# Kernel optimization log

Hardware: AMD Instinct MI355X
Metric: run time of the kernel (lower is better)

Reference implementation:

```python
import jax, jax.numpy as jnp
import numpy as np

STRIDE = 4
EPS = 1e-12  # guards sqrt grad at exactly-zero distance (weight[0] is all zeros)


def rbf_conv(x, w, stride=STRIDE):
    # x: (N, 1, H, W); w: (O, kh, kw). Computes per-window cdist to all O
    # prototype filters, then gauss RBF with std = unbiased std of the (N, O)
    # distance matrix at each window position (matches torch.std(dist)).
    O, kh, kw = w.shape
    patches = jax.lax.conv_general_dilated_patches(
        x, (kh, kw), (stride, stride), 'VALID')      # (N, kh*kw, oh, ow)
    p = jnp.transpose(patches, (0, 2, 3, 1))          # (N, oh, ow, P)
    wf = w.reshape(O, -1)                              # (O, P)
    d2 = (jnp.sum(p * p, -1)[..., None] + jnp.sum(wf * wf, -1)
          - 2.0 * jnp.einsum('nhwp,op->nhwo', p, wf))
    dist = jnp.sqrt(jnp.maximum(d2, 0.0) + EPS)       # (N, oh, ow, O)
    std = jnp.std(dist, axis=(0, 3), ddof=1, keepdims=True)  # per window pos
    out = jnp.exp(-0.5 * (dist / std) ** 2)           # gauss RBF
    return jnp.transpose(out, (0, 3, 1, 2))           # (N, O, oh, ow)


def crelu(x, b):
    return x * (x >= b).astype(x.dtype)


def sfm(x, shape, next_kernel, filt, alpha0=0.9):
    # get_RM: (N, C, h_in, w_in) -> (B, h, w, C) regrouping, then alpha-weighted
    # patch pooling over `filt`, emitting (B*h'*w', 1, kh_next, kw_next).
    h, w = shape
    f0, f1 = filt
    C = x.shape[1]
    rm = jnp.transpose(x, (0, 2, 3, 1)).reshape(-1, h, w, C)
    seq = jnp.arange(f0 * f1, dtype=x.dtype)[::-1]       # flipped sequence
    alpha = jnp.tile((alpha0 ** seq).reshape(f0, f1), (h // f0, w // f1))
    out = rm * alpha[None, :, :, None]
    out = out.reshape(-1, h // f0, f0, w // f1, f1, C).mean(axis=(2, 4))
    return out.reshape(-1, 1, *next_kernel)


def channel_forward(xc, w1, w2, w3, w4, cb):
    y = rbf_conv(xc, w1)                       # (B, 100, 6, 6)
    y = crelu(y, cb[0])
    y = sfm(y, (6, 6), (10, 10), (2, 2))       # (B*9, 1, 10, 10)
    y = rbf_conv(y, w2)                        # (B*9, 225, 1, 1)
    y = crelu(y, cb[1])
    y = sfm(y, (3, 3), (15, 15), (1, 3))       # (B*3, 1, 15, 15)
    y = rbf_conv(y, w3)                        # (B*3, 625, 1, 1)
    y = crelu(y, cb[2])
    y = sfm(y, (3, 1), (25, 25), (3, 1))       # (B, 1, 25, 25)
    y = rbf_conv(y, w4)                        # (B, 1225, 1, 1)
    y = crelu(y, cb[3])
    return y


def forward(x, w1, w2, w3, w4, fc_w, fc_b, crelu_bias):
    B = x.shape[0]
    feats = [channel_forward(x[:, c:c + 1], w1[c], w2[c], w3[c], w4[c], crelu_bias)
             for c in range(x.shape[1])]        # fixed loop over 3 color channels
    out = jnp.concatenate(feats, axis=1).reshape(B, -1)  # (B, 3*1225)
    return out @ fc_w.T + fc_b


def setup_inputs() -> dict:
    key = jax.random.key(0)
    ks = jax.random.split(key, 8)

    def kaiming_u(k, shape):
        fan_in = int(np.prod(shape[2:]))        # 1*kh*kw, matches torch
        bound = float(np.sqrt(1.0 / fan_in))    # kaiming_uniform(a=sqrt(5))
        w = jax.random.uniform(k, shape, jnp.float32, -bound, bound)
        return w.at[:, 0].set(0.0)              # torch init zeros filter 0

    B = 4096
    return {
        'x': jax.random.uniform(ks[0], (B, 3, 28, 28), jnp.float32),
        'w1': kaiming_u(ks[1], (3, 100, 5, 5)),
        'w2': kaiming_u(ks[2], (3, 225, 10, 10)),
        'w3': kaiming_u(ks[3], (3, 625, 15, 15)),
        'w4': kaiming_u(ks[4], (3, 1225, 25, 25)),
        'fc_w': jax.random.normal(ks[5], (10, 3 * 1225), jnp.float32) * 0.016,
        'fc_b': jnp.zeros((10,), jnp.float32),
        'crelu_bias': jnp.array([0.4, 0.1, 0.01, 0.01], jnp.float32),
    }


def reference(x, w1, w2, w3, w4, fc_w, fc_b, crelu_bias):
    return forward(x, w1, w2, w3, w4, fc_w, fc_b, crelu_bias)
```

## Files before the change

### kernel.cpp

```cpp
#include <hip/hip_runtime.h>


typedef unsigned short u16;
typedef short bf16x8 __attribute__((ext_vector_type(8)));
typedef float f32x4 __attribute__((ext_vector_type(4)));

#define STRIPES 64
#define ACC_L2 0
#define ACC_L3 128
#define ACC_L4 256
#define ACC_TOTAL 384

__device__ __forceinline__ u16 f2bf(float f) {
  unsigned int u = __float_as_uint(f);
  unsigned int r = (u + 0x7fffu + ((u >> 16) & 1u)) >> 16;
  return (u16)r;
}
__device__ __forceinline__ float bf2f(u16 h) {
  return __uint_as_float(((unsigned int)h) << 16);
}
__device__ __forceinline__ float fexp(float x) { return __expf(x); }
__device__ __forceinline__ float fsqrt(float x) { return __builtin_amdgcn_sqrtf(x); }
__device__ __forceinline__ void gload16(const void* g, const void* l) {
  __builtin_amdgcn_global_load_lds(
      (const __attribute__((address_space(1))) unsigned int*)g,
      (__attribute__((address_space(3))) unsigned int*)l, 16, 0, 0);
}

__global__ void zero_acc_kernel(double* __restrict__ acc, int n) {
  int i = blockIdx.x * blockDim.x + threadIdx.x;
  if (i < n) acc[i] = 0.0;
}

__global__ __launch_bounds__(128) void w_prep(
    const float* __restrict__ W, int O, int K, int Opad, int Kp,
    u16* __restrict__ hi, u16* __restrict__ lo, float* __restrict__ wn)
{
  __shared__ float red[2];
  int o = blockIdx.x, cc = blockIdx.y, t = threadIdx.x;
  const float* src = W + ((size_t)cc * O + o) * K;
  u16* dh = hi + ((size_t)cc * Opad + o) * Kp;
  u16* dl = lo + ((size_t)cc * Opad + o) * Kp;
  float p = 0.f;
  for (int k = t; k < Kp; k += 128) {
    float v = (o < O && k < K) ? src[k] : 0.f;
    u16 h = f2bf(v);
    u16 l = f2bf(v - bf2f(h));
    dh[k] = h; dl[k] = l;
    p = fmaf(v, v, p);
  }
  for (int off = 32; off; off >>= 1) p += __shfl_down(p, off, 64);
  if ((t & 63) == 0) red[t >> 6] = p;
  __syncthreads();
  if (t == 0) wn[(size_t)cc * Opad + o] = red[0] + red[1];
}

__global__ __launch_bounds__(256) void l1_gemm_d2(
    const float* __restrict__ x, int c0,
    const u16* __restrict__ W1h, const u16* __restrict__ W1l,
    const float* __restrict__ w1n, float* __restrict__ dist1, int sD1c,
    float* __restrict__ part, int sPartc, int NBLK)
{
  __shared__ __align__(16) u16 sm[16384];
  __shared__ float img[1568];
  __shared__ float pnsm[512];
  __shared__ float pnloc[128];
  __shared__ float sqred[4][36][2];
  const int t = threadIdx.x;
  const int w = t >> 6, lane = t & 63;
  const int b0 = blockIdx.x * 2;
  const int zi = blockIdx.y, c = c0 + zi;
  const u16* Wh = W1h + (size_t)c * 4096;
  const u16* Wl = W1l + (size_t)c * 4096;
  const float* wn = w1n + (size_t)c * 128;
  dist1 += (size_t)zi * sD1c;
  part  += (size_t)zi * sPartc;

  {
    const int kk = (w & 3) * 8;
#pragma unroll
    for (int u = 0; u < 2; ++u) {
      const size_t gb = (size_t)(u * 64 + lane) * 32 + kk;
      const int ls = ((w & 3) * 128 + u * 64) * 8;
      gload16(Wh + gb, sm + 8192 + ls);
      gload16(Wl + gb, sm + 12288 + ls);
    }
  }
#pragma unroll
  for (int im = 0; im < 2; ++im) {
    if (t < 196)
      ((float4*)(img + im * 784))[t] =
          ((const float4*)(x + ((size_t)(b0 + im) * 3 + c) * 784))[t];
  }
  __syncthreads();
  for (int s = t; s < 512; s += 256) {
    int q = s >> 7, row = s & 127;
    int im = row >> 6, pr = row & 63;
    int pi = pr / 6, pj = pr - pi * 6;
    const float* ib = img + im * 784 + pi * 4 * 28 + pj * 4;
    float v[8]; float pn = 0.f;
#pragma unroll
    for (int e = 0; e < 8; ++e) {
      int k = q * 8 + e;
      float val = 0.f;
      if (pr < 36 && k < 25) { int r = k / 5, ss = k - r * 5; val = ib[r * 28 + ss]; }
      v[e] = val; pn = fmaf(val, val, pn);
    }
    u16 hi8[8], lo8[8];
#pragma unroll
    for (int e = 0; e < 8; ++e) {
      u16 h = f2bf(v[e]); hi8[e] = h; lo8[e] = f2bf(v[e] - bf2f(h));
    }
    *(bf16x8*)(sm + (q * 128 + row) * 8) = *(bf16x8*)hi8;
    *(bf16x8*)(sm + 4096 + (q * 128 + row) * 8) = *(bf16x8*)lo8;
    pnsm[s] = pn;
  }
  asm volatile("s_waitcnt vmcnt(0)" ::: "memory");
  __syncthreads();
  if (t < 128) pnloc[t] = pnsm[t] + pnsm[128 + t] + pnsm[256 + t] + pnsm[384 + t];

  const int wr = w >> 1, wc = w & 1;
  const int q4 = lane >> 4, r16 = lane & 15;
  f32x4 accv[4][4];
#pragma unroll
  for (int i = 0; i < 4; ++i)
#pragma unroll
    for (int j = 0; j < 4; ++j) accv[i][j] = (f32x4){0.f, 0.f, 0.f, 0.f};

  bf16x8 Ah[4], Al[4], Bh[4], Bl[4];
#pragma unroll
  for (int i = 0; i < 4; ++i) {
    int ao = (q4 * 128 + wr * 64 + i * 16 + r16) * 8;
    int bo = (q4 * 128 + wc * 64 + i * 16 + r16) * 8;
    Ah[i] = *(const bf16x8*)(sm + ao);
    Al[i] = *(const bf16x8*)(sm + 4096 + ao);
    Bh[i] = *(const bf16x8*)(sm + 8192 + bo);
    Bl[i] = *(const bf16x8*)(sm + 12288 + bo);
  }
#pragma unroll
  for (int j = 0; j < 4; ++j) {
#pragma unroll
    for (int i = 0; i < 4; ++i)
      accv[i][j] = __builtin_amdgcn_mfma_f32_16x16x32_bf16(Ah[i], Bh[j], accv[i][j], 0, 0, 0);
#pragma unroll
    for (int i = 0; i < 4; ++i)
      accv[i][j] = __builtin_amdgcn_mfma_f32_16x16x32_bf16(Al[i], Bh[j], accv[i][j], 0, 0, 0);
#pragma unroll
    for (int i = 0; i < 4; ++i)
      accv[i][j] = __builtin_amdgcn_mfma_f32_16x16x32_bf16(Ah[i], Bl[j], accv[i][j], 0, 0, 0);
  }
  __syncthreads();

  int colv[4]; float wnv[4];
#pragma unroll
  for (int j = 0; j < 4; ++j) {
    colv[j] = wc * 64 + j * 16 + r16;
    wnv[j] = (colv[j] < 100) ? wn[colv[j]] : 0.f;
  }
#pragma unroll
  for (int i = 0; i < 4; ++i) {
#pragma unroll
    for (int r = 0; r < 4; ++r) {
      int pos = i * 16 + q4 * 4 + r;
      if (pos < 36) {
        float pn = pnloc[wr * 64 + pos];
        float* drow = dist1 + ((size_t)(b0 + wr) * 36 + pos) * 100;
        float sl = 0.f, ql = 0.f;
#pragma unroll
        for (int j = 0; j < 4; ++j) {
          if (colv[j] < 100) {
            float d2 = pn + wnv[j] - 2.f * accv[i][j][r];
            float d2c = fmaxf(d2, 0.f) + 1e-12f;
            drow[colv[j]] = d2c;
            sl += fsqrt(d2c); ql += d2c;
          }
        }
#pragma unroll
        for (int off = 8; off; off >>= 1) {
          sl += __shfl_xor(sl, off, 64);
          ql += __shfl_xor(ql, off, 64);
        }
        if (r16 == 0) { sqred[w][pos][0] = sl; sqred[w][pos][1] = ql; }
      }
    }
  }
  __syncthreads();
  if (t < 36) {
    float ss = sqred[0][t][0] + sqred[1][t][0] + sqred[2][t][0] + sqred[3][t][0];
    float qq = sqred[0][t][1] + sqred[1][t][1] + sqred[2][t][1] + sqred[3][t][1];
    part[(size_t)t * NBLK + blockIdx.x] = ss;
    part[(size_t)(36 + t) * NBLK + blockIdx.x] = qq;
  }
}

__global__ __launch_bounds__(256) void l1_part_fin(
    const float* __restrict__ part, int sPartc, float* __restrict__ inv36, int sInvc,
    double n, int NBLK)
{
  __shared__ double sh[8];
  int pos = blockIdx.x, zi = blockIdx.y, t = threadIdx.x;
  part += (size_t)zi * sPartc; inv36 += (size_t)zi * sInvc;
  double s = 0.0, q = 0.0;
  for (int b = t; b < NBLK; b += 256) {
    s += part[(size_t)pos * NBLK + b];
    q += part[(size_t)(36 + pos) * NBLK + b];
  }
  for (int off = 32; off; off >>= 1) {
    s += __shfl_down(s, off, 64);
    q += __shfl_down(q, off, 64);
  }
  if ((t & 63) == 0) { sh[(t >> 6) * 2] = s; sh[(t >> 6) * 2 + 1] = q; }
  __syncthreads();
  if (t == 0) {
    s = sh[0] + sh[2] + sh[4] + sh[6];
    q = sh[1] + sh[3] + sh[5] + sh[7];
    double var = (q - s * s / n) / (n - 1.0);
    inv36[pos] = var > 0.0 ? (float)(0.5 / var) : __builtin_inff();
  }
}

__global__ __launch_bounds__(128) void l1_sfm_lite(
    const float* __restrict__ d1, int sD1c,
    const float* __restrict__ inv36, int sInvc, const float* __restrict__ cb,
    u16* __restrict__ Xhi, u16* __restrict__ Xlo, float* __restrict__ xn,
    int sXc, int sxnc)
{
  __shared__ float inv_s[36];
  __shared__ float xnsm[9][2];
  int b = blockIdx.x, zi = blockIdx.y, t = threadIdx.x;
  d1 += (size_t)zi * sD1c; inv36 += (size_t)zi * sInvc;
  Xhi += (size_t)zi * sXc; Xlo += (size_t)zi * sXc; xn += (size_t)zi * sxnc;
  if (t < 36) inv_s[t] = inv36[t];
  __syncthreads();
  const float* db = d1 + (size_t)b * 3600;
  float bias = cb[0];
  int wv = t >> 6;
#pragma unroll
  for (int IJ = 0; IJ < 9; ++IJ) {
    const int I = IJ / 3, J = IJ - I * 3;
    const int p00 = 12 * I + 2 * J;
    float v = 0.f;
    if (t < 100) {
      float e00 = fexp(-db[p00 * 100 + t] * inv_s[p00]);
      float e01 = fexp(-db[(p00 + 1) * 100 + t] * inv_s[p00 + 1]);
      float e10 = fexp(-db[(p00 + 6) * 100 + t] * inv_s[p00 + 6]);
      float e11 = fexp(-db[(p00 + 7) * 100 + t] * inv_s[p00 + 7]);
      e00 = (e00 >= bias) ? e00 : 0.f;
      e01 = (e01 >= bias) ? e01 : 0.f;
      e10 = (e10 >= bias) ? e10 : 0.f;
      e11 = (e11 >= bias) ? e11 : 0.f;
      v = 0.25f * (fmaf(0.729f, e00, 0.81f * e01) + fmaf(0.9f, e10, e11));
    }
    size_t xrow = (size_t)b * 9 + IJ;
    u16 h = f2bf(v);
    u16 l = f2bf(v - bf2f(h));
    Xhi[xrow * 128 + t] = h;
    Xlo[xrow * 128 + t] = l;
    float p = v * v;
    for (int off = 32; off; off >>= 1) p += __shfl_down(p, off, 64);
    if ((t & 63) == 0) xnsm[IJ][wv] = p;
  }
  __syncthreads();
  if (t < 9) xn[(size_t)b * 9 + t] = xnsm[t][0] + xnsm[t][1];
}

__global__ __launch_bounds__(512, 2) void gemm_dist_pipe(
    const u16* __restrict__ Xhi, const u16* __restrict__ Xlo,
    const u16* __restrict__ Whi, const u16* __restrict__ Wlo,
    const float* __restrict__ xn, const float* __restrict__ wn,
    float* __restrict__ dist, int O, int Kp,
    double* __restrict__ acc, int accbase, int c0,
    int sXc, int sWc, int sxnc, int swnc, int sdistc)
{
  __shared__ __align__(16) u16 sm[65536];
  int zi = blockIdx.z, c = c0 + zi;
  Xhi += (size_t)zi * sXc; Xlo += (size_t)zi * sXc;
  Whi += (size_t)c * sWc;  Wlo += (size_t)c * sWc;
  xn += (size_t)zi * sxnc; wn += (size_t)c * swnc;
  dist += (size_t)zi * sdistc;
  acc += (size_t)c * ACC_TOTAL;

  const int t = threadIdx.x;
  const int w = t >> 6, lane = t & 63;
  const int wr = w >> 1, wc = w & 1;
  const int sq = w & 3, half = w >> 2;
  const int m0 = blockIdx.x * 256, o0 = blockIdx.y * 256;
  const int q4 = lane >> 4, r16 = lane & 15;
  const int nsteps = Kp / 32;

  f32x4 accv[4][8];
#pragma unroll
  for (int i = 0; i < 4; ++i)
#pragma unroll
    for (int j = 0; j < 8; ++j) accv[i][j] = (f32x4){0.f, 0.f, 0.f, 0.f};

  auto stageA = [&](int buf, int ks) {
    const int kk = ks * 32 + sq * 8;
    u16* base = sm + buf * 32768;
#pragma unroll
    for (int u = 0; u < 2; ++u) {
      const int row = half * 128 + u * 64 + lane;
      const size_t ga = (size_t)(m0 + row) * Kp + kk;
      const int ls = (sq * 256 + half * 128 + u * 64) * 8;
      gload16(Xhi + ga, base + ls);
      gload16(Xlo + ga, base + 8192 + ls);
    }
  };
  auto stageB = [&](int buf, int ks) {
    const int kk = ks * 32 + sq * 8;
    u16* base = sm + buf * 32768;
#pragma unroll
    for (int u = 0; u < 2; ++u) {
      const int row = half * 128 + u * 64 + lane;
      const size_t gb = (size_t)(o0 + row) * Kp + kk;
      const int ls = (sq * 256 + half * 128 + u * 64) * 8;
      gload16(Whi + gb, base + 16384 + ls);
      gload16(Wlo + gb, base + 24576 + ls);
    }
  };

  stageA(0, 0);
  stageB(0, 0);
  for (int ks = 0; ks < nsteps; ++ks) {
    const u16* base = sm + (ks & 1) * 32768;
    asm volatile("s_waitcnt vmcnt(2)\n\ts_barrier" ::: "memory");
    if (ks + 1 < nsteps) stageA((ks + 1) & 1, ks + 1);

    bf16x8 Ah[4], Al[4];
#pragma unroll
    for (int i = 0; i < 4; ++i) {
      int ao = (q4 * 256 + wr * 64 + i * 16 + r16) * 8;
      Ah[i] = *(const bf16x8*)(base + ao);
      Al[i] = *(const bf16x8*)(base + 8192 + ao);
    }
    __builtin_amdgcn_s_setprio(1);
#pragma unroll
    for (int j = 0; j < 4; ++j) {
      int bo = (q4 * 256 + wc * 128 + j * 16 + r16) * 8;
      bf16x8 Bh = *(const bf16x8*)(base + 16384 + bo);
      bf16x8 Bl = *(const bf16x8*)(base + 24576 + bo);
#pragma unroll
      for (int i = 0; i < 4; ++i)
        accv[i][j] = __builtin_amdgcn_mfma_f32_16x16x32_bf16(Ah[i], Bh, accv[i][j], 0, 0, 0);
#pragma unroll
      for (int i = 0; i < 4; ++i)
        accv[i][j] = __builtin_amdgcn_mfma_f32_16x16x32_bf16(Al[i], Bh, accv[i][j], 0, 0, 0);
#pragma unroll
      for (int i = 0; i < 4; ++i)
        accv[i][j] = __builtin_amdgcn_mfma_f32_16x16x32_bf16(Ah[i], Bl, accv[i][j], 0, 0, 0);
    }
    __builtin_amdgcn_s_setprio(0);

    if (ks + 1 < nsteps) {
      asm volatile("s_waitcnt vmcnt(4)\n\ts_barrier" ::: "memory");
      stageB((ks + 1) & 1, ks + 1);
    } else {
      asm volatile("s_waitcnt vmcnt(0)\n\ts_barrier" ::: "memory");
    }
    __builtin_amdgcn_s_setprio(1);
#pragma unroll
    for (int j = 4; j < 8; ++j) {
      int bo = (q4 * 256 + wc * 128 + j * 16 + r16) * 8;
      bf16x8 Bh = *(const bf16x8*)(base + 16384 + bo);
      bf16x8 Bl = *(const bf16x8*)(base + 24576 + bo);
#pragma unroll
      for (int i = 0; i < 4; ++i)
        accv[i][j] = __builtin_amdgcn_mfma_f32_16x16x32_bf16(Ah[i], Bh, accv[i][j], 0, 0, 0);
#pragma unroll
      for (int i = 0; i < 4; ++i)
        accv[i][j] = __builtin_amdgcn_mfma_f32_16x16x32_bf16(Al[i], Bh, accv[i][j], 0, 0, 0);
#pragma unroll
      for (int i = 0; i < 4; ++i)
        accv[i][j] = __builtin_amdgcn_mfma_f32_16x16x32_bf16(Ah[i], Bl, accv[i][j], 0, 0, 0);
    }
    __builtin_amdgcn_s_setprio(0);
  }

  double s = 0.0, qd = 0.0;
#pragma unroll
  for (int i = 0; i < 4; ++i) {
    const int mb = m0 + wr * 64 + i * 16 + q4 * 4;
    float xnv[4];
#pragma unroll
    for (int r = 0; r < 4; ++r) xnv[r] = xn[mb + r];
    float sf = 0.f, qf = 0.f;
#pragma unroll
    for (int j = 0; j < 8; ++j) {
      const int o = o0 + wc * 128 + j * 16 + r16;
      if (o < O) {
        const float wnv = wn[o];
#pragma unroll
        for (int r = 0; r < 4; ++r) {
          float d2 = xnv[r] + wnv - 2.f * accv[i][j][r];
          float d2c = fmaxf(d2, 0.f) + 1e-12f;
          dist[(size_t)(mb + r) * O + o] = d2c;
          sf += fsqrt(d2c); qf += d2c;
        }
      }
    }
    s += sf; qd += qf;
  }
  for (int off = 32; off; off >>= 1) {
    s += __shfl_down(s, off, 64);
    qd += __shfl_down(qd, off, 64);
  }
  double* redsm = (double*)(sm + (nsteps & 1) * 32768);
  if (lane == 0) { redsm[w * 2] = s; redsm[w * 2 + 1] = qd; }
  __syncthreads();
  if (t == 0) {
    s = 0.0; qd = 0.0;
#pragma unroll
    for (int ww = 0; ww < 8; ++ww) { s += redsm[ww * 2]; qd += redsm[ww * 2 + 1]; }
    int stripe = (blockIdx.x + blockIdx.y * gridDim.x) & (STRIPES - 1);
    atomicAdd(&acc[accbase + stripe * 2], s);
    atomicAdd(&acc[accbase + stripe * 2 + 1], qd);
  }
}

__device__ __forceinline__ float block_inv_from_acc(
    const double* __restrict__ acc, int base, double n, float* sh)
{
  __syncthreads();
  int t = threadIdx.x;
  if (t < 64) {
    double s = acc[base + 2 * t], q = acc[base + 2 * t + 1];
    for (int off = 32; off; off >>= 1) {
      s += __shfl_down(s, off, 64);
      q += __shfl_down(q, off, 64);
    }
    if (t == 0) {
      double var = (q - s * s / n) / (n - 1.0);
      *sh = var > 0.0 ? (float)(0.5 / var) : __builtin_inff();
    }
  }
  __syncthreads();
  return *sh;
}

__global__ __launch_bounds__(256) void l2_sfm(
    const float* __restrict__ dist2, const double* __restrict__ acc, double n,
    const float* __restrict__ cb, u16* __restrict__ Xhi, u16* __restrict__ Xlo,
    float* __restrict__ xn, int c0, int sdistc, int sXc, int sxnc)
{
  __shared__ float shinv;
  __shared__ float red[4];
  int zi = blockIdx.z, c = c0 + zi;
  dist2 += (size_t)zi * sdistc;
  Xhi += (size_t)zi * sXc; Xlo += (size_t)zi * sXc; xn += (size_t)zi * sxnc;
  float inv = block_inv_from_acc(acc + (size_t)c * ACC_TOTAL, ACC_L2, n, &shinv);
  int b = blockIdx.x, u = blockIdx.y, ch = threadIdx.x;
  float bias = cb[1];
  float v = 0.f;
  if (ch < 225) {
    const float av[3] = {0.81f, 0.9f, 1.0f};
    float a = 0.f;
#pragma unroll
    for (int vv = 0; vv < 3; ++vv) {
      float d2 = dist2[((size_t)b * 9 + u * 3 + vv) * 225 + ch];
      float e = fexp(-d2 * inv);
      e = (e >= bias) ? e : 0.f;
      a = fmaf(e, av[vv], a);
    }
    v = a * (1.f / 3.f);
  }
  size_t row = (size_t)b * 3 + u;
  u16 h = f2bf(v);
  u16 l = f2bf(v - bf2f(h));
  Xhi[row * 256 + ch] = h;
  Xlo[row * 256 + ch] = l;
  float p = v * v;
  for (int off = 32; off; off >>= 1) p += __shfl_down(p, off, 64);
  if ((ch & 63) == 0) red[ch >> 6] = p;
  __syncthreads();
  if (ch == 0) xn[row] = red[0] + red[1] + red[2] + red[3];
}

__global__ __launch_bounds__(256) void l3_sfm(
    const float* __restrict__ dist3, const double* __restrict__ acc, double n,
    const float* __restrict__ cb, u16* __restrict__ Xhi, u16* __restrict__ Xlo,
    float* __restrict__ xn, int c0, int sdistc, int sXc, int sxnc)
{
  __shared__ float shinv;
  __shared__ float red[4];
  int zi = blockIdx.y, c = c0 + zi;
  dist3 += (size_t)zi * sdistc;
  Xhi += (size_t)zi * sXc; Xlo += (size_t)zi * sXc; xn += (size_t)zi * sxnc;
  float inv = block_inv_from_acc(acc + (size_t)c * ACC_TOTAL, ACC_L3, n, &shinv);
  int b = blockIdx.x, t = threadIdx.x;
  float bias = cb[2];
  const float au[3] = {0.81f, 0.9f, 1.0f};
  float p = 0.f;
  for (int ch = t; ch < 640; ch += 256) {
    float v = 0.f;
    if (ch < 625) {
      float a = 0.f;
#pragma unroll
      for (int u = 0; u < 3; ++u) {
        float d2 = dist3[((size_t)b * 3 + u) * 625 + ch];
        float e = fexp(-d2 * inv);
        e = (e >= bias) ? e : 0.f;
        a = fmaf(e, au[u], a);
      }
      v = a * (1.f / 3.f);
    }
    u16 h = f2bf(v);
    u16 l = f2bf(v - bf2f(h));
    Xhi[(size_t)b * 640 + ch] = h;
    Xlo[(size_t)b * 640 + ch] = l;
    p = fmaf(v, v, p);
  }
  for (int off = 32; off; off >>= 1) p += __shfl_down(p, off, 64);
  if ((t & 63) == 0) red[t >> 6] = p;
  __syncthreads();
  if (t == 0) xn[b] = red[0] + red[1] + red[2] + red[3];
}

__global__ __launch_bounds__(128) void fc_acc(
    const float* __restrict__ dist4, const double* __restrict__ acc, double n,
    const float* __restrict__ cb, const float* __restrict__ fcw,
    const float* __restrict__ fcb, float* __restrict__ out,
    int c0, int nc, int sdistc)
{
  __shared__ float shinv;
  int b = blockIdx.x, t = threadIdx.x;
  float bias = cb[3];
  float p[10];
#pragma unroll
  for (int k = 0; k < 10; ++k) p[k] = 0.f;
  for (int zi = 0; zi < nc; ++zi) {
    int c = c0 + zi;
    float inv = block_inv_from_acc(acc + (size_t)c * ACC_TOTAL, ACC_L4, n, &shinv);
    const float* d4 = dist4 + (size_t)zi * sdistc;
    for (int j = t; j < 1225; j += 128) {
      float d2 = d4[(size_t)b * 1225 + j];
      float v = fexp(-d2 * inv);
      v = (v >= bias) ? v : 0.f;
#pragma unroll
      for (int k = 0; k < 10; ++k) p[k] = fmaf(v, fcw[k * 3675 + c * 1225 + j], p[k]);
    }
  }
#pragma unroll
  for (int k = 0; k < 10; ++k)
    for (int off = 32; off; off >>= 1) p[k] += __shfl_down(p[k], off, 64);
  __shared__ float red[2][10];
  int wave = t >> 6;
  if ((t & 63) == 0) {
#pragma unroll
    for (int k = 0; k < 10; ++k) red[wave][k] = p[k];
  }
  __syncthreads();
  if (t < 10) {
    float v = red[0][t] + red[1][t];
    if (c0 == 0) out[(size_t)b * 10 + t] = fcb[t] + v;
    else         out[(size_t)b * 10 + t] += v;
  }
}

extern "C" void kernel_launch(void* const* d_in, const int* in_sizes, int n_in,
                              void* d_out, int out_size, void* d_ws, size_t ws_size,
                              hipStream_t stream) {
  const float* x   = (const float*)d_in[0];
  const float* w1  = (const float*)d_in[1];
  const float* w2  = (const float*)d_in[2];
  const float* w3  = (const float*)d_in[3];
  const float* w4  = (const float*)d_in[4];
  const float* fcw = (const float*)d_in[5];
  const float* fcb = (const float*)d_in[6];
  const float* cb  = (const float*)d_in[7];
  float* out = (float*)d_out;
  const int B = in_sizes[0] / (3 * 28 * 28);
  const int M2 = B * 9, M3 = B * 3;
  const int NB = B / 2;

  const size_t W2SZ = 256 * 128, W3SZ = 768 * 256, W4SZ = (size_t)1280 * 640;
  const size_t WTOT = 3 * (W2SZ + W3SZ + W4SZ);

  int tier;
  u16 *Xbase, *Whi, *Wlo, *W1h, *W1l;
  float *wn, *w1n, *xn, *inv36, *part;
  double* accd;
  float* Sf;
  for (tier = 0; tier < 3; ++tier) {
    size_t cur = 0;
    char* basep = (char*)d_ws;
    auto take = [&](size_t bytes) {
      void* r = basep + cur;
      cur = (cur + bytes + 255) & ~(size_t)255;
      return r;
    };
    int nc = (tier <= 1) ? 3 : 1;
    int ncL1 = (tier == 0) ? 3 : 1;
    size_t Ssz = (size_t)M2 * 225 * 4 * nc;
    size_t d1sz = (size_t)B * 3600 * 4 * ncL1;
    if (d1sz > Ssz) Ssz = d1sz;
    Sf = (float*)take(Ssz);
    Xbase = (u16*)take((size_t)M2 * 128 * 2 * 2 * nc);
    Whi = (u16*)take(WTOT * 2); Wlo = (u16*)take(WTOT * 2);
    W1h = (u16*)take(12288 * 2); W1l = (u16*)take(12288 * 2);
    wn  = (float*)take(3 * (256 + 768 + 1280) * 4);
    w1n = (float*)take(384 * 4);
    xn    = (float*)take((size_t)M2 * 4 * nc);
    inv36 = (float*)take(40 * 4 * ncL1);
    part  = (float*)take((size_t)72 * NB * 4 * ncL1);
    accd  = (double*)take(3 * ACC_TOTAL * 8);
    if (cur <= ws_size || tier == 2) break;
  }
  const int nc = (tier <= 1) ? 3 : 1;
  const bool batL1 = (tier == 0);

  const int sX2c   = (nc == 3) ? M2 * 128 * 2 : 0;
  const int sX3c   = (nc == 3) ? M3 * 256 * 2 : 0;
  const int sX4c   = (nc == 3) ? B * 640 * 2 : 0;
  const int sD2c   = (nc == 3) ? M2 * 225 : 0;
  const int sD3c   = (nc == 3) ? M3 * 625 : 0;
  const int sD4c   = (nc == 3) ? B * 1225 : 0;
  const int sXn2c  = (nc == 3) ? M2 : 0;
  const int sXn3c  = (nc == 3) ? M3 : 0;
  const int sXn4c  = (nc == 3) ? B : 0;
  const int sD1c   = batL1 ? B * 3600 : 0;
  const int sPartc = batL1 ? 72 * NB : 0;
  const int sInvL1 = batL1 ? 40 : 0;

  u16* x2hi = Xbase;   u16* x2lo = Xbase + (size_t)M2 * 128;
  u16* x3hi = Xbase;   u16* x3lo = Xbase + (size_t)M3 * 256;
  u16* x4hi = Xbase;   u16* x4lo = Xbase + (size_t)B * 640;
  u16* Whi2 = Whi;                 u16* Wlo2 = Wlo;                 float* wn2 = wn;
  u16* Whi3 = Whi + 3 * W2SZ;      u16* Wlo3 = Wlo + 3 * W2SZ;      float* wn3 = wn + 3 * 256;
  u16* Whi4 = Whi + 3 * (W2SZ + W3SZ); u16* Wlo4 = Wlo + 3 * (W2SZ + W3SZ);
  float* wn4 = wn + 3 * (256 + 768);

  zero_acc_kernel<<<(3 * ACC_TOTAL + 255) / 256, 256, 0, stream>>>(accd, 3 * ACC_TOTAL);
  w_prep<<<dim3(128, 3),  128, 0, stream>>>(w1, 100, 25,  128, 32,  W1h,  W1l,  w1n);
  w_prep<<<dim3(256, 3),  128, 0, stream>>>(w2, 225, 100, 256, 128, Whi2, Wlo2, wn2);
  w_prep<<<dim3(768, 3),  128, 0, stream>>>(w3, 625, 225, 768, 256, Whi3, Wlo3, wn3);
  w_prep<<<dim3(1280, 3), 128, 0, stream>>>(w4, 1225, 625, 1280, 640, Whi4, Wlo4, wn4);

  for (int c0 = 0; c0 < 3; c0 += nc) {
    if (batL1) {
      l1_gemm_d2<<<dim3(NB, 3), 256, 0, stream>>>(x, 0, W1h, W1l, w1n, Sf, sD1c,
                                                  part, sPartc, NB);
      l1_part_fin<<<dim3(36, 3), 256, 0, stream>>>(part, sPartc, inv36, sInvL1,
                                                   (double)B * 100.0, NB);
      l1_sfm_lite<<<dim3(B, 3), 128, 0, stream>>>(
          Sf, sD1c, inv36, sInvL1, cb, x2hi, x2lo, xn, sX2c, sXn2c);
    } else {
      for (int ci = 0; ci < nc; ++ci) {
        int c = c0 + ci;
        l1_gemm_d2<<<dim3(NB, 1), 256, 0, stream>>>(x, c, W1h, W1l, w1n, Sf, 0,
                                                    part, 0, NB);
        l1_part_fin<<<dim3(36, 1), 256, 0, stream>>>(part, 0, inv36, 0,
                                                     (double)B * 100.0, NB);
        l1_sfm_lite<<<dim3(B, 1), 128, 0, stream>>>(
            Sf, 0, inv36, 0, cb, x2hi + (size_t)ci * sX2c, x2lo + (size_t)ci * sX2c,
            xn + (size_t)ci * sXn2c, 0, 0);
      }
    }

    gemm_dist_pipe<<<dim3(M2 / 256, 1, nc), 512, 0, stream>>>(
        x2hi, x2lo, Whi2, Wlo2, xn, wn2, Sf, 225, 128, accd, ACC_L2, c0,
        sX2c, (int)W2SZ, sXn2c, 256, sD2c);
    l2_sfm<<<dim3(B, 3, nc), 256, 0, stream>>>(
        Sf, accd, (double)M2 * 225.0, cb, x3hi, x3lo, xn, c0, sD2c, sX3c, sXn3c);

    gemm_dist_pipe<<<dim3(M3 / 256, 3, nc), 512, 0, stream>>>(
        x3hi, x3lo, Whi3, Wlo3, xn, wn3, Sf, 625, 256, accd, ACC_L3, c0,
        sX3c, (int)W3SZ, sXn3c, 768, sD3c);
    l3_sfm<<<dim3(B, nc), 256, 0, stream>>>(
        Sf, accd, (double)M3 * 625.0, cb, x4hi, x4lo, xn, c0, sD3c, sX4c, sXn4c);

    gemm_dist_pipe<<<dim3(B / 256, 5, nc), 512, 0, stream>>>(
        x4hi, x4lo, Whi4, Wlo4, xn, wn4, Sf, 1225, 640, accd, ACC_L4, c0,
        sX4c, (int)W4SZ, sXn4c, 1280, sD4c);
    fc_acc<<<B, 128, 0, stream>>>(
        Sf, accd, (double)B * 1225.0, cb, fcw, fcb, out, c0, nc, sD4c);
  }
}
```

Baseline: 490.9 us.

## Recompute layer-1 distances in SFM kernel instead of storing to global memory

The first layer-1 kernel now only computes the per-position sum and sum-of-squares statistics and no longer writes the full (B,36,100) squared-distance tensor. A new fused SFM kernel recomputes the small bf16-split MFMA GEMM per pair of images, stages the distances in shared memory, then applies the RBF, crelu and pooling. This trades a second pass of cheap GEMM work for removing a large global write and read of the distance buffer, and shrinks the workspace requirement.

```diff
diff --git a/kernel.cpp b/kernel.cpp
--- a/kernel.cpp
+++ b/kernel.cpp
@@ -55,10 +55,10 @@
   if (t == 0) wn[(size_t)cc * Opad + o] = red[0] + red[1];
 }
 
-__global__ __launch_bounds__(256) void l1_gemm_d2(
+__global__ __launch_bounds__(256) void l1_gemm_sq(
     const float* __restrict__ x, int c0,
     const u16* __restrict__ W1h, const u16* __restrict__ W1l,
-    const float* __restrict__ w1n, float* __restrict__ dist1, int sD1c,
+    const float* __restrict__ w1n,
     float* __restrict__ part, int sPartc, int NBLK)
 {
   __shared__ __align__(16) u16 sm[16384];
@@ -73,8 +73,7 @@
   const u16* Wh = W1h + (size_t)c * 4096;
   const u16* Wl = W1l + (size_t)c * 4096;
   const float* wn = w1n + (size_t)c * 128;
-  dist1 += (size_t)zi * sD1c;
-  part  += (size_t)zi * sPartc;
+  part += (size_t)zi * sPartc;
 
   {
     const int kk = (w & 3) * 8;
@@ -164,14 +163,12 @@
       int pos = i * 16 + q4 * 4 + r;
       if (pos < 36) {
         float pn = pnloc[wr * 64 + pos];
-        float* drow = dist1 + ((size_t)(b0 + wr) * 36 + pos) * 100;
         float sl = 0.f, ql = 0.f;
 #pragma unroll
         for (int j = 0; j < 4; ++j) {
           if (colv[j] < 100) {
             float d2 = pn + wnv[j] - 2.f * accv[i][j][r];
             float d2c = fmaxf(d2, 0.f) + 1e-12f;
-            drow[colv[j]] = d2c;
             sl += fsqrt(d2c); ql += d2c;
           }
         }
@@ -219,49 +216,167 @@
   }
 }
 
-__global__ __launch_bounds__(128) void l1_sfm_lite(
-    const float* __restrict__ d1, int sD1c,
+__global__ __launch_bounds__(256) void l1_sfm_fused(
+    const float* __restrict__ x, int c0,
+    const u16* __restrict__ W1h, const u16* __restrict__ W1l,
+    const float* __restrict__ w1n,
     const float* __restrict__ inv36, int sInvc, const float* __restrict__ cb,
     u16* __restrict__ Xhi, u16* __restrict__ Xlo, float* __restrict__ xn,
     int sXc, int sxnc)
 {
+  __shared__ __align__(16) u16 sm[16384];
+  __shared__ float img[1568];
+  __shared__ float pnsm[512];
+  __shared__ float pnloc[128];
   __shared__ float inv_s[36];
-  __shared__ float xnsm[9][2];
-  int b = blockIdx.x, zi = blockIdx.y, t = threadIdx.x;
-  d1 += (size_t)zi * sD1c; inv36 += (size_t)zi * sInvc;
+  __shared__ float xnsm[2][9][2];
+  const int t = threadIdx.x;
+  const int w = t >> 6, lane = t & 63;
+  const int b0 = blockIdx.x * 2;
+  const int zi = blockIdx.y, c = c0 + zi;
+  const u16* Wh = W1h + (size_t)c * 4096;
+  const u16* Wl = W1l + (size_t)c * 4096;
+  const float* wn = w1n + (size_t)c * 128;
+  inv36 += (size_t)zi * sInvc;
   Xhi += (size_t)zi * sXc; Xlo += (size_t)zi * sXc; xn += (size_t)zi * sxnc;
-  if (t < 36) inv_s[t] = inv36[t];
-  __syncthreads();
-  const float* db = d1 + (size_t)b * 3600;
+
+  {
+    const int kk = (w & 3) * 8;
+#pragma unroll
+    for (int u = 0; u < 2; ++u) {
+      const size_t gb = (size_t)(u * 64 + lane) * 32 + kk;
+      const int ls = ((w & 3) * 128 + u * 64) * 8;
+      gload16(Wh + gb, sm + 8192 + ls);
+      gload16(Wl + gb, sm + 12288 + ls);
+    }
+  }
+#pragma unroll
+  for (int im = 0; im < 2; ++im) {
+    if (t < 196)
+      ((float4*)(img + im * 784))[t] =
+          ((const float4*)(x + ((size_t)(b0 + im) * 3 + c) * 784))[t];
+  }
+  __syncthreads();
+  for (int s = t; s < 512; s += 256) {
+    int q = s >> 7, row = s & 127;
+    int im = row >> 6, pr = row & 63;
+    int pi = pr / 6, pj = pr - pi * 6;
+    const float* ib = img + im * 784 + pi * 4 * 28 + pj * 4;
+    float v[8]; float pn = 0.f;
+#pragma unroll
+    for (int e = 0; e < 8; ++e) {
+      int k = q * 8 + e;
+      float val = 0.f;
+      if (pr < 36 && k < 25) { int r = k / 5, ss = k - r * 5; val = ib[r * 28 + ss]; }
+      v[e] = val; pn = fmaf(val, val, pn);
+    }
+    u16 hi8[8], lo8[8];
+#pragma unroll
+    for (int e = 0; e < 8; ++e) {
+      u16 h = f2bf(v[e]); hi8[e] = h; lo8[e] = f2bf(v[e] - bf2f(h));
+    }
+    *(bf16x8*)(sm + (q * 128 + row) * 8) = *(bf16x8*)hi8;
+    *(bf16x8*)(sm + 4096 + (q * 128 + row) * 8) = *(bf16x8*)lo8;
+    pnsm[s] = pn;
+  }
+  asm volatile("s_waitcnt vmcnt(0)" ::: "memory");
+  __syncthreads();
+  if (t < 128) pnloc[t] = pnsm[t] + pnsm[128 + t] + pnsm[256 + t] + pnsm[384 + t];
+  if (t >= 200 && t < 236) inv_s[t - 200] = inv36[t - 200];
+
+  const int wr = w >> 1, wc = w & 1;
+  const int q4 = lane >> 4, r16 = lane & 15;
+  f32x4 accv[4][4];
+#pragma unroll
+  for (int i = 0; i < 4; ++i)
+#pragma unroll
+    for (int j = 0; j < 4; ++j) accv[i][j] = (f32x4){0.f, 0.f, 0.f, 0.f};
+
+  bf16x8 Ah[4], Al[4], Bh[4], Bl[4];
+#pragma unroll
+  for (int i = 0; i < 4; ++i) {
+    int ao = (q4 * 128 + wr * 64 + i * 16 + r16) * 8;
+    int bo = (q4 * 128 + wc * 64 + i * 16 + r16) * 8;
+    Ah[i] = *(const bf16x8*)(sm + ao);
+    Al[i] = *(const bf16x8*)(sm + 4096 + ao);
+    Bh[i] = *(const bf16x8*)(sm + 8192 + bo);
+    Bl[i] = *(const bf16x8*)(sm + 12288 + bo);
+  }
+#pragma unroll
+  for (int j = 0; j < 4; ++j) {
+#pragma unroll
+    for (int i = 0; i < 4; ++i)
+      accv[i][j] = __builtin_amdgcn_mfma_f32_16x16x32_bf16(Ah[i], Bh[j], accv[i][j], 0, 0, 0);
+#pragma unroll
+    for (int i = 0; i < 4; ++i)
+      accv[i][j] = __builtin_amdgcn_mfma_f32_16x16x32_bf16(Al[i], Bh[j], accv[i][j], 0, 0, 0);
+#pragma unroll
+    for (int i = 0; i < 4; ++i)
+      accv[i][j] = __builtin_amdgcn_mfma_f32_16x16x32_bf16(Ah[i], Bl[j], accv[i][j], 0, 0, 0);
+  }
+  __syncthreads();
+
+  float* smf = (float*)sm;
+  {
+    int colv[4]; float wnv[4];
+#pragma unroll
+    for (int j = 0; j < 4; ++j) {
+      colv[j] = wc * 64 + j * 16 + r16;
+      wnv[j] = (colv[j] < 100) ? wn[colv[j]] : 0.f;
+    }
+#pragma unroll
+    for (int i = 0; i < 4; ++i) {
+#pragma unroll
+      for (int r = 0; r < 4; ++r) {
+        int pos = i * 16 + q4 * 4 + r;
+        if (pos < 36) {
+          float pn = pnloc[wr * 64 + pos];
+#pragma unroll
+          for (int j = 0; j < 4; ++j) {
+            if (colv[j] < 100) {
+              float d2 = pn + wnv[j] - 2.f * accv[i][j][r];
+              smf[(wr * 36 + pos) * 100 + colv[j]] = fmaxf(d2, 0.f) + 1e-12f;
+            }
+          }
+        }
+      }
+    }
+  }
+  __syncthreads();
+
+  const int ch = t & 127, im = t >> 7;
+  const float* dbase = smf + im * 3600;
   float bias = cb[0];
-  int wv = t >> 6;
 #pragma unroll
   for (int IJ = 0; IJ < 9; ++IJ) {
     const int I = IJ / 3, J = IJ - I * 3;
     const int p00 = 12 * I + 2 * J;
     float v = 0.f;
-    if (t < 100) {
-      float e00 = fexp(-db[p00 * 100 + t] * inv_s[p00]);
-      float e01 = fexp(-db[(p00 + 1) * 100 + t] * inv_s[p00 + 1]);
-      float e10 = fexp(-db[(p00 + 6) * 100 + t] * inv_s[p00 + 6]);
-      float e11 = fexp(-db[(p00 + 7) * 100 + t] * inv_s[p00 + 7]);
+    if (ch < 100) {
+      float e00 = fexp(-dbase[p00 * 100 + ch] * inv_s[p00]);
+      float e01 = fexp(-dbase[(p00 + 1) * 100 + ch] * inv_s[p00 + 1]);
+      float e10 = fexp(-dbase[(p00 + 6) * 100 + ch] * inv_s[p00 + 6]);
+      float e11 = fexp(-dbase[(p00 + 7) * 100 + ch] * inv_s[p00 + 7]);
       e00 = (e00 >= bias) ? e00 : 0.f;
       e01 = (e01 >= bias) ? e01 : 0.f;
       e10 = (e10 >= bias) ? e10 : 0.f;
       e11 = (e11 >= bias) ? e11 : 0.f;
       v = 0.25f * (fmaf(0.729f, e00, 0.81f * e01) + fmaf(0.9f, e10, e11));
     }
-    size_t xrow = (size_t)b * 9 + IJ;
+    size_t xrow = (size_t)(b0 + im) * 9 + IJ;
     u16 h = f2bf(v);
     u16 l = f2bf(v - bf2f(h));
-    Xhi[xrow * 128 + t] = h;
-    Xlo[xrow * 128 + t] = l;
+    Xhi[xrow * 128 + ch] = h;
+    Xlo[xrow * 128 + ch] = l;
     float p = v * v;
     for (int off = 32; off; off >>= 1) p += __shfl_down(p, off, 64);
-    if ((t & 63) == 0) xnsm[IJ][wv] = p;
-  }
-  __syncthreads();
-  if (t < 9) xn[(size_t)b * 9 + t] = xnsm[t][0] + xnsm[t][1];
+    if ((t & 63) == 0) xnsm[im][IJ][(t >> 6) & 1] = p;
+  }
+  __syncthreads();
+  if (t < 18) {
+    int i2 = t / 9, IJ = t - i2 * 9;
+    xn[(size_t)(b0 + i2) * 9 + IJ] = xnsm[i2][IJ][0] + xnsm[i2][IJ][1];
+  }
 }
 
 __global__ __launch_bounds__(512, 2) void gemm_dist_pipe(
@@ -591,8 +706,6 @@
     int nc = (tier <= 1) ? 3 : 1;
     int ncL1 = (tier == 0) ? 3 : 1;
     size_t Ssz = (size_t)M2 * 225 * 4 * nc;
-    size_t d1sz = (size_t)B * 3600 * 4 * ncL1;
-    if (d1sz > Ssz) Ssz = d1sz;
     Sf = (float*)take(Ssz);
     Xbase = (u16*)take((size_t)M2 * 128 * 2 * 2 * nc);
     Whi = (u16*)take(WTOT * 2); Wlo = (u16*)take(WTOT * 2);
@@ -617,7 +730,6 @@
   const int sXn2c  = (nc == 3) ? M2 : 0;
   const int sXn3c  = (nc == 3) ? M3 : 0;
   const int sXn4c  = (nc == 3) ? B : 0;
-  const int sD1c   = batL1 ? B * 3600 : 0;
   const int sPartc = batL1 ? 72 * NB : 0;
   const int sInvL1 = batL1 ? 40 : 0;
 
@@ -637,21 +749,22 @@
 
   for (int c0 = 0; c0 < 3; c0 += nc) {
     if (batL1) {
-      l1_gemm_d2<<<dim3(NB, 3), 256, 0, stream>>>(x, 0, W1h, W1l, w1n, Sf, sD1c,
+      l1_gemm_sq<<<dim3(NB, 3), 256, 0, stream>>>(x, 0, W1h, W1l, w1n,
                                                   part, sPartc, NB);
       l1_part_fin<<<dim3(36, 3), 256, 0, stream>>>(part, sPartc, inv36, sInvL1,
                                                    (double)B * 100.0, NB);
-      l1_sfm_lite<<<dim3(B, 3), 128, 0, stream>>>(
-          Sf, sD1c, inv36, sInvL1, cb, x2hi, x2lo, xn, sX2c, sXn2c);
+      l1_sfm_fused<<<dim3(NB, 3), 256, 0, stream>>>(
+          x, 0, W1h, W1l, w1n, inv36, sInvL1, cb, x2hi, x2lo, xn, sX2c, sXn2c);
     } else {
       for (int ci = 0; ci < nc; ++ci) {
         int c = c0 + ci;
-        l1_gemm_d2<<<dim3(NB, 1), 256, 0, stream>>>(x, c, W1h, W1l, w1n, Sf, 0,
+        l1_gemm_sq<<<dim3(NB, 1), 256, 0, stream>>>(x, c, W1h, W1l, w1n,
                                                     part, 0, NB);
         l1_part_fin<<<dim3(36, 1), 256, 0, stream>>>(part, 0, inv36, 0,
                                                      (double)B * 100.0, NB);
-        l1_sfm_lite<<<dim3(B, 1), 128, 0, stream>>>(
-            Sf, 0, inv36, 0, cb, x2hi + (size_t)ci * sX2c, x2lo + (size_t)ci * sX2c,
+        l1_sfm_fused<<<dim3(NB, 1), 256, 0, stream>>>(
+            x, c, W1h, W1l, w1n, inv36, 0, cb,
+            x2hi + (size_t)ci * sX2c, x2lo + (size_t)ci * sX2c,
             xn + (size_t)ci * sXn2c, 0, 0);
       }
     }
```

Result: slower. 502.1 us (+2.3%).
